# Kernel optimization log

Hardware: AMD Instinct MI355X
Metric: run time of the kernel (lower is better)

## Reference

```python
import jax, jax.numpy as jnp
import numpy as np


def setup_inputs() -> dict:
    key = jax.random.key(0)
    k1, k2 = jax.random.split(key)
    decoder_output = jax.random.normal(k1, (8, 2048, 128), dtype=jnp.float32)
    encoder_output = jax.random.normal(k2, (8, 4096, 128), dtype=jnp.float32)
    return {"decoder_output": decoder_output, "encoder_output": encoder_output}


def reference(decoder_output, encoder_output):
    # Unscaled Luong (general dot) attention.
    # scores: [B, Tq, Tk] = dec [B,Tq,D] . enc [B,Tk,D]^T
    scores = jnp.einsum('bqd,bkd->bqk', decoder_output, encoder_output)
    attention = jax.nn.softmax(scores, axis=-1)
    # context: [B, Tq, D] = attn [B,Tq,Tk] . enc [B,Tk,D]
    context = jnp.einsum('bqk,bkd->bqd', attention, encoder_output)
    return (context, attention)
```

## Files before the change

kernel.cpp:

```cpp
#include <hip/hip_runtime.h>

using f16   = _Float16;
using f16x4 = __attribute__((ext_vector_type(4))) _Float16;
using f16x8 = __attribute__((ext_vector_type(8))) _Float16;
using f32x4 = __attribute__((ext_vector_type(4))) float;

#define NBATCH 8
#define TQ 2048
#define TK 4096
#define DD 128
#define QBLK 32
#define KBLK 128
#define NT (TK / KBLK)
#define CTX_ELEMS ((size_t)NBATCH * TQ * DD)
#define PWLD 56
#define CTLD 132

__device__ __forceinline__ int koff(int t, int d) {
    const int blk = ((t >> 2) & 3) ^ ((d >> 4) & 3);
    return (t >> 4) * 2304 + (d >> 4) * 288 + blk * 72 + (t & 3) * 16 + (d & 15);
}

__device__ __forceinline__ f16x4 ds_read_tr16(unsigned addr) {
    f16x4 d;
    asm volatile("ds_read_b64_tr_b16 %0, %1" : "=v"(d) : "v"(addr));
    return d;
}

__device__ __forceinline__ void stage_tile(f16* Kt, const float* src, int tid) {
    #pragma unroll
    for (int i = 0; i < 8; ++i) {
        const int idx = tid + (i << 9);
        const int t = idx >> 5;
        const int d = (idx & 31) << 2;
        const float4 v = *(const float4*)(src + t * DD + d);
        f16x4 h;
        h[0] = (f16)v.x; h[1] = (f16)v.y; h[2] = (f16)v.z; h[3] = (f16)v.w;
        *(f16x4*)&Kt[koff(t, d)] = h;
    }
}

__global__ __launch_bounds__(512, 4)
void luong_attn_kernel(const float* __restrict__ dec,
                       const float* __restrict__ enc,
                       float* __restrict__ out) {
    __shared__ __align__(16) char LDSbuf[36864 + 8 * 16 * PWLD * 2 + 512];
    f16*   Kt     = (f16*)LDSbuf;
    f16*   PwAll  = (f16*)(LDSbuf + 36864);
    float* Zbuf   = (float*)(LDSbuf + 36864 + 8 * 16 * PWLD * 2);

    const int tid  = threadIdx.x;
    const int wid  = tid >> 6;
    const int lane = tid & 63;
    const int lo   = lane & 15;
    const int g    = lane >> 4;
    const int qg   = wid & 1;
    const int th   = wid >> 1;

    const int b     = blockIdx.x & 7;
    const int qbase = (blockIdx.x >> 3) * QBLK;

    const float* encB = enc + ((size_t)b * TK) * DD;
    float* attn = out + CTX_ELEMS + ((size_t)b * TQ + qbase) * TK;

    const float* qp = dec + ((size_t)b * TQ + qbase + qg * 16 + lo) * DD;
    f16x8 qf[4];
    #pragma unroll
    for (int kk = 0; kk < 4; ++kk) {
        const float4 x = *(const float4*)(qp + kk * 32 + g * 8);
        const float4 y = *(const float4*)(qp + kk * 32 + g * 8 + 4);
        f16x8 h;
        h[0] = (f16)x.x; h[1] = (f16)x.y; h[2] = (f16)x.z; h[3] = (f16)x.w;
        h[4] = (f16)y.x; h[5] = (f16)y.y; h[6] = (f16)y.z; h[7] = (f16)y.w;
        qf[kk] = h;
    }

    float Zp[4] = {0.f, 0.f, 0.f, 0.f};
    #pragma unroll 1
    for (int tile = 0; tile < NT; ++tile) {
        stage_tile(Kt, encB + (size_t)tile * KBLK * DD, tid);
        __syncthreads();
        f32x4 S[2];
        #pragma unroll
        for (int f = 0; f < 2; ++f) { f32x4 z = {0.f, 0.f, 0.f, 0.f}; S[f] = z; }
        #pragma unroll
        for (int f = 0; f < 2; ++f) {
            const int t = th * 32 + f * 16 + lo;
            #pragma unroll
            for (int kk = 0; kk < 4; ++kk) {
                const f16x8 bf = *(const f16x8*)&Kt[koff(t, kk * 32 + g * 8)];
                S[f] = __builtin_amdgcn_mfma_f32_16x16x32_f16(qf[kk], bf, S[f], 0, 0, 0);
            }
        }
        __syncthreads();
        #pragma unroll
        for (int r = 0; r < 4; ++r)
            Zp[r] += __expf(S[0][r]) + __expf(S[1][r]);
    }

    #pragma unroll
    for (int r = 0; r < 4; ++r) {
        Zp[r] += __shfl_xor(Zp[r], 1);
        Zp[r] += __shfl_xor(Zp[r], 2);
        Zp[r] += __shfl_xor(Zp[r], 4);
        Zp[r] += __shfl_xor(Zp[r], 8);
    }
    if (lo == 0) {
        #pragma unroll
        for (int r = 0; r < 4; ++r) Zbuf[wid * 16 + 4 * g + r] = Zp[r];
    }
    __syncthreads();
    float iz[4];
    #pragma unroll
    for (int r = 0; r < 4; ++r) {
        float z = 0.f;
        #pragma unroll
        for (int t4 = 0; t4 < 4; ++t4) z += Zbuf[(t4 * 2 + qg) * 16 + 4 * g + r];
        iz[r] = 1.0f / z;
    }
    __syncthreads();

    f32x4 ctx[8];
    #pragma unroll
    for (int n = 0; n < 8; ++n) { f32x4 z = {0.f, 0.f, 0.f, 0.f}; ctx[n] = z; }

    f16* Pw = PwAll + wid * 16 * PWLD;
    const unsigned KtBase = (unsigned)(size_t)&Kt[0];
    const int t0 = th * 32 + g * 8;

    #pragma unroll 1
    for (int tile = 0; tile < NT; ++tile) {
        stage_tile(Kt, encB + (size_t)tile * KBLK * DD, tid);
        __syncthreads();

        f32x4 S[2];
        #pragma unroll
        for (int f = 0; f < 2; ++f) { f32x4 z = {0.f, 0.f, 0.f, 0.f}; S[f] = z; }
        #pragma unroll
        for (int f = 0; f < 2; ++f) {
            const int t = th * 32 + f * 16 + lo;
            #pragma unroll
            for (int kk = 0; kk < 4; ++kk) {
                const f16x8 bf = *(const f16x8*)&Kt[koff(t, kk * 32 + g * 8)];
                S[f] = __builtin_amdgcn_mfma_f32_16x16x32_f16(qf[kk], bf, S[f], 0, 0, 0);
            }
        }

        #pragma unroll
        for (int f = 0; f < 2; ++f) {
            const int tloc = f * 16 + lo;
            #pragma unroll
            for (int r = 0; r < 4; ++r) {
                const int q = 4 * g + r;
                const float p = __expf(S[f][r]) * iz[r];
                __builtin_nontemporal_store(
                    p, attn + (size_t)(qg * 16 + q) * TK + tile * KBLK + th * 32 + tloc);
                Pw[q * PWLD + tloc] = (f16)p;
            }
        }
        asm volatile("" ::: "memory");

        const f16x8 pa = *(const f16x8*)&Pw[lo * PWLD + g * 8];
        #pragma unroll
        for (int nh = 0; nh < 2; ++nh) {
            f16x4 tr0[4], tr1[4];
            #pragma unroll
            for (int n4 = 0; n4 < 4; ++n4) {
                const int n = nh * 4 + n4;
                const int blk0 = ((t0 >> 2) & 3) ^ (n & 3);
                const int blk1 = (((t0 + 4) >> 2) & 3) ^ (n & 3);
                const unsigned a0 =
                    KtBase + (unsigned)(((t0 >> 4) * 2304 + n * 288 + blk0 * 72) * 2) + lo * 8;
                const unsigned a1 =
                    KtBase + (unsigned)(((t0 >> 4) * 2304 + n * 288 + blk1 * 72) * 2) + lo * 8;
                tr0[n4] = ds_read_tr16(a0);
                tr1[n4] = ds_read_tr16(a1);
            }
            asm volatile("s_waitcnt lgkmcnt(0)" ::: "memory");
            __builtin_amdgcn_sched_barrier(0);
            #pragma unroll
            for (int n4 = 0; n4 < 4; ++n4) {
                f16x8 vb;
                vb[0] = tr0[n4][0]; vb[1] = tr0[n4][1]; vb[2] = tr0[n4][2]; vb[3] = tr0[n4][3];
                vb[4] = tr1[n4][0]; vb[5] = tr1[n4][1]; vb[6] = tr1[n4][2]; vb[7] = tr1[n4][3];
                ctx[nh * 4 + n4] =
                    __builtin_amdgcn_mfma_f32_16x16x32_f16(pa, vb, ctx[nh * 4 + n4], 0, 0, 0);
            }
        }
        __syncthreads();
    }

    float* CT = (float*)LDSbuf;
    const int q32 = qg * 16 + 4 * g;
    if (th >= 2) {
        #pragma unroll
        for (int n = 0; n < 8; ++n)
            #pragma unroll
            for (int r = 0; r < 4; ++r)
                CT[((th - 2) * 32 + q32 + r) * CTLD + n * 16 + lo] = ctx[n][r];
    }
    __syncthreads();
    if (th < 2) {
        #pragma unroll
        for (int n = 0; n < 8; ++n)
            #pragma unroll
            for (int r = 0; r < 4; ++r)
                ctx[n][r] += CT[(th * 32 + q32 + r) * CTLD + n * 16 + lo];
    }
    __syncthreads();
    if (th == 1) {
        #pragma unroll
        for (int n = 0; n < 8; ++n)
            #pragma unroll
            for (int r = 0; r < 4; ++r)
                CT[(q32 + r) * CTLD + n * 16 + lo] = ctx[n][r];
    }
    __syncthreads();
    if (th == 0) {
        #pragma unroll
        for (int n = 0; n < 8; ++n)
            #pragma unroll
            for (int r = 0; r < 4; ++r)
                out[((size_t)b * TQ + qbase + q32 + r) * DD + n * 16 + lo] =
                    ctx[n][r] + CT[(q32 + r) * CTLD + n * 16 + lo];
    }
}

extern "C" void kernel_launch(void* const* d_in, const int* in_sizes, int n_in,
                              void* d_out, int out_size, void* d_ws, size_t ws_size,
                              hipStream_t stream) {
    (void)in_sizes; (void)n_in; (void)out_size; (void)d_ws; (void)ws_size;
    const float* dec = (const float*)d_in[0];
    const float* enc = (const float*)d_in[1];
    float* out = (float*)d_out;
    dim3 grid(NBATCH * (TQ / QBLK));
    dim3 block(512);
    hipLaunchKernelGGL(luong_attn_kernel, grid, block, 0, stream, dec, enc, out);
}
```

Measured before the change: 144.5 us.

## Prefetch next encoder tile into registers and vectorize attention stores via LDS

Encoder tiles are loaded into registers one iteration ahead, so global load latency overlaps with the MFMA work in both passes. Attention probabilities are no longer written with scalar strided stores. They are read back from the per-wave f16 LDS buffer and written as contiguous 16-byte nontemporal stores. This reduces store transactions, but the stored attention values now carry f16 rounding, and the prefetch raises register pressure.

```diff
diff --git a/kernel.cpp b/kernel.cpp
--- a/kernel.cpp
+++ b/kernel.cpp
@@ -27,15 +27,22 @@
     return d;
 }
 
-__device__ __forceinline__ void stage_tile(f16* Kt, const float* src, int tid) {
+__device__ __forceinline__ void load_tile(float4* pre, const float* src, int tid) {
+    #pragma unroll
+    for (int i = 0; i < 8; ++i) {
+        const int idx = tid + (i << 9);
+        pre[i] = *(const float4*)(src + (idx >> 5) * DD + ((idx & 31) << 2));
+    }
+}
+__device__ __forceinline__ void write_tile(const float4* pre, f16* Kt, int tid) {
     #pragma unroll
     for (int i = 0; i < 8; ++i) {
         const int idx = tid + (i << 9);
         const int t = idx >> 5;
         const int d = (idx & 31) << 2;
-        const float4 v = *(const float4*)(src + t * DD + d);
         f16x4 h;
-        h[0] = (f16)v.x; h[1] = (f16)v.y; h[2] = (f16)v.z; h[3] = (f16)v.w;
+        h[0] = (f16)pre[i].x; h[1] = (f16)pre[i].y;
+        h[2] = (f16)pre[i].z; h[3] = (f16)pre[i].w;
         *(f16x4*)&Kt[koff(t, d)] = h;
     }
 }
@@ -45,9 +52,9 @@
                        const float* __restrict__ enc,
                        float* __restrict__ out) {
     __shared__ __align__(16) char LDSbuf[36864 + 8 * 16 * PWLD * 2 + 512];
-    f16*   Kt     = (f16*)LDSbuf;
-    f16*   PwAll  = (f16*)(LDSbuf + 36864);
-    float* Zbuf   = (float*)(LDSbuf + 36864 + 8 * 16 * PWLD * 2);
+    f16*   Kt    = (f16*)LDSbuf;
+    f16*   PwAll = (f16*)(LDSbuf + 36864);
+    float* Zbuf  = (float*)(LDSbuf + 36864 + 8 * 16 * PWLD * 2);
 
     const int tid  = threadIdx.x;
     const int wid  = tid >> 6;
@@ -75,11 +82,16 @@
         qf[kk] = h;
     }
 
+    float4 pre[8];
+    load_tile(pre, encB, tid);
+
     float Zp[4] = {0.f, 0.f, 0.f, 0.f};
     #pragma unroll 1
     for (int tile = 0; tile < NT; ++tile) {
-        stage_tile(Kt, encB + (size_t)tile * KBLK * DD, tid);
-        __syncthreads();
+        write_tile(pre, Kt, tid);
+        if (tile + 1 < NT) load_tile(pre, encB + (size_t)(tile + 1) * KBLK * DD, tid);
+        __syncthreads();
+
         f32x4 S[2];
         #pragma unroll
         for (int f = 0; f < 2; ++f) { f32x4 z = {0.f, 0.f, 0.f, 0.f}; S[f] = z; }
@@ -93,10 +105,13 @@
             }
         }
         __syncthreads();
+
         #pragma unroll
         for (int r = 0; r < 4; ++r)
             Zp[r] += __expf(S[0][r]) + __expf(S[1][r]);
     }
+
+    load_tile(pre, encB, tid);
 
     #pragma unroll
     for (int r = 0; r < 4; ++r) {
@@ -130,7 +145,8 @@
 
     #pragma unroll 1
     for (int tile = 0; tile < NT; ++tile) {
-        stage_tile(Kt, encB + (size_t)tile * KBLK * DD, tid);
+        write_tile(pre, Kt, tid);
+        if (tile + 1 < NT) load_tile(pre, encB + (size_t)(tile + 1) * KBLK * DD, tid);
         __syncthreads();
 
         f32x4 S[2];
@@ -150,13 +166,8 @@
         for (int f = 0; f < 2; ++f) {
             const int tloc = f * 16 + lo;
             #pragma unroll
-            for (int r = 0; r < 4; ++r) {
-                const int q = 4 * g + r;
-                const float p = __expf(S[f][r]) * iz[r];
-                __builtin_nontemporal_store(
-                    p, attn + (size_t)(qg * 16 + q) * TK + tile * KBLK + th * 32 + tloc);
-                Pw[q * PWLD + tloc] = (f16)p;
-            }
+            for (int r = 0; r < 4; ++r)
+                Pw[(4 * g + r) * PWLD + tloc] = (f16)(__expf(S[f][r]) * iz[r]);
         }
         asm volatile("" ::: "memory");
 
@@ -187,6 +198,18 @@
                     __builtin_amdgcn_mfma_f32_16x16x32_f16(pa, vb, ctx[nh * 4 + n4], 0, 0, 0);
             }
         }
+
+        {
+            const int qq  = lane >> 2;
+            const int grp = lane & 3;
+            const f16x8 pr = *(const f16x8*)&Pw[qq * PWLD + grp * 8];
+            f32x4 a0, a1;
+            a0[0] = (float)pr[0]; a0[1] = (float)pr[1]; a0[2] = (float)pr[2]; a0[3] = (float)pr[3];
+            a1[0] = (float)pr[4]; a1[1] = (float)pr[5]; a1[2] = (float)pr[6]; a1[3] = (float)pr[7];
+            float* dst = attn + (size_t)(qg * 16 + qq) * TK + tile * KBLK + th * 32 + grp * 8;
+            __builtin_nontemporal_store(a0, (f32x4*)dst);
+            __builtin_nontemporal_store(a1, (f32x4*)(dst + 4));
+        }
         __syncthreads();
     }
 
```

Measured after the change: 189.0 us. +30.8%, slower.
